# Optimization experiments

Hardware: AMD Instinct MI355X
Metric: run time of the kernel (lower is better)

The kernel has to match this reference:

```python
import jax, jax.numpy as jnp
import numpy as np

DIM = 2048
DIM_HEADS = 64
NUM_HEADS = DIM // DIM_HEADS  # 32


def setup_inputs() -> dict:
    key = jax.random.key(0)
    k1, k2, k3, k4 = jax.random.split(key, 4)
    B, N = 2, 2048
    x = jax.random.normal(k1, (B, N, DIM), dtype=jnp.float32)
    freqs = jax.random.normal(k2, (N, DIM_HEADS), dtype=jnp.float32)
    W_qkv = jax.random.normal(k3, (3 * DIM, DIM), dtype=jnp.float32) * 0.02
    W_out = jax.random.normal(k4, (DIM, DIM), dtype=jnp.float32) * 0.02
    return {"x": x, "freqs": freqs, "W_qkv": W_qkv, "W_out": W_out}


def _rotate_half(x):
    # split last dim into two halves (j=2), return cat(-x2, x1)
    x1, x2 = jnp.split(x, 2, axis=-1)
    return jnp.concatenate([-x2, x1], axis=-1)


def _apply_rotary_pos_emb(t, freqs, scale=1.0):
    # t: [b, h, n, d]; freqs: [n, rot_dim]; rotary math in float32
    out_dtype = t.dtype
    rot_dim = freqs.shape[-1]
    seq_len = t.shape[-2]
    freqs = freqs.astype(jnp.float32)[-seq_len:, :]  # [n, rot_dim]
    t = t.astype(jnp.float32)
    t_rot, t_unrot = t[..., :rot_dim], t[..., rot_dim:]
    t_rot = t_rot * jnp.cos(freqs) * scale + _rotate_half(t_rot) * jnp.sin(freqs) * scale
    return jnp.concatenate([t_rot.astype(out_dtype), t_unrot.astype(out_dtype)], axis=-1)


def reference(x, freqs, W_qkv, W_out):
    B, N, _ = x.shape
    h, d = NUM_HEADS, DIM_HEADS
    # fused QKV projection (Linear, no bias): x @ W_qkv.T
    qkv = jnp.einsum('bnc,fc->bnf', x, W_qkv)  # [B, N, 3*DIM]
    q, k, v = jnp.split(qkv, 3, axis=-1)
    q = q.reshape(B, N, h, d).transpose(0, 2, 1, 3)  # [B, h, N, d]
    k = k.reshape(B, N, h, d).transpose(0, 2, 1, 3)
    v = v.reshape(B, N, h, d).transpose(0, 2, 1, 3)
    # equal q/k seq lens -> ratio = 1, same freqs for both
    q = _apply_rotary_pos_emb(q, freqs)
    k = _apply_rotary_pos_emb(k, freqs)
    # scaled dot-product attention (non-causal)
    scale = 1.0 / np.sqrt(d).astype(np.float32)
    scores = jnp.einsum('bhqd,bhkd->bhqk', q, k) * scale
    attn = jax.nn.softmax(scores, axis=-1)
    out = jnp.einsum('bhqk,bhkd->bhqd', attn, v)
    out = out.transpose(0, 2, 1, 3).reshape(B, N, h * d)  # [B, N, DIM]
    return jnp.einsum('bnc,oc->bno', out, W_out)
```

## Files before the change

### kernel.cpp

```cpp
#include <hip/hip_runtime.h>

#define DIMC 2048
#define NSEQ 2048
#define NBATCH 2
#define NH 32
#define DH 64
#define BHEADS (NBATCH*NH)
#define MROWS (NBATCH*NSEQ)
#define NQKV (3*DIMC)

typedef __attribute__((ext_vector_type(8))) short short8;
typedef __attribute__((ext_vector_type(4))) float f32x4;
typedef __attribute__((ext_vector_type(4))) unsigned int uint4v;
typedef __attribute__((ext_vector_type(2))) unsigned int u32x2;

static __device__ __forceinline__ unsigned short f2bf(float f) {
  union { float f; unsigned int u; } v; v.f = f;
  unsigned int r = (v.u + 0x7FFFu + ((v.u >> 16) & 1u)) >> 16;
  return (unsigned short)r;
}

static __device__ __forceinline__ unsigned int cvt_pk_bf16(float lo, float hi) {
  unsigned int r;
  asm("v_cvt_pk_bf16_f32 %0, %1, %2" : "=v"(r) : "v"(lo), "v"(hi));
  return r;
}

#define BAR()    __builtin_amdgcn_s_barrier()
#define FENCE()  asm volatile("" ::: "memory")
#define LGKM0()  asm volatile("s_waitcnt lgkmcnt(0)" ::: "memory")
#define VM(n)    asm volatile("s_waitcnt vmcnt(" #n ")" ::: "memory")

__global__ __launch_bounds__(256) void cvt_bf16(const float* __restrict__ in,
                                                unsigned short* __restrict__ out,
                                                int n8) {
  int i = blockIdx.x * blockDim.x + threadIdx.x;
  int stride = gridDim.x * blockDim.x;
  for (; i < n8; i += stride) {
    const float4* p = (const float4*)in + (size_t)i * 2;
    float4 a = p[0], b = p[1];
    union { unsigned short u[8]; uint4v v; } o;
    o.u[0] = f2bf(a.x); o.u[1] = f2bf(a.y); o.u[2] = f2bf(a.z); o.u[3] = f2bf(a.w);
    o.u[4] = f2bf(b.x); o.u[5] = f2bf(b.y); o.u[6] = f2bf(b.z); o.u[7] = f2bf(b.w);
    *((uint4v*)out + i) = o.v;
  }
}

__global__ __launch_bounds__(256) void build_cs(const float* __restrict__ freqs,
                                                float2* __restrict__ cs, int n) {
  int i = blockIdx.x * blockDim.x + threadIdx.x;
  if (i < n) { float f = freqs[i]; cs[i] = make_float2(cosf(f), sinf(f)); }
}

#define QSCALE 0.18033688011112042f
#define SLOT 24576

template<int EPI>
__global__ __launch_bounds__(512, 1) void gemm128(
    const unsigned short* __restrict__ A,
    const unsigned short* __restrict__ Bm,
    int Kdim, int Ncols,
    float* __restrict__ Cout,
    unsigned short* __restrict__ qo, unsigned short* __restrict__ ko,
    unsigned short* __restrict__ vo, const float2* __restrict__ cs)
{
  extern __shared__ char Lds[];
  const int t = threadIdx.x;
  const int w = t >> 6, lane = t & 63, lr = lane & 15, g = lane >> 4;
  const int wm = w >> 2, wn = w & 3;

  const int nx = gridDim.x;
  int orig = blockIdx.y * nx + blockIdx.x;
  int cpx = (nx * gridDim.y) >> 3;
  int id = (orig & 7) * cpx + (orig >> 3);
  const int m0 = (id / nx) * 128;
  const int n0 = (id % nx) * 256;

  const int rowt = t >> 2, colt = (t & 3) * 8;
  const unsigned short* Abase = A + (size_t)(m0 + rowt) * Kdim + colt;
  const unsigned short* Bbase = Bm + (size_t)(n0 + rowt) * Kdim + colt;
  char* dstw = Lds + w * 1024;

  auto STAGE = [&](int sbuf, int T) {
    const unsigned short* sa = Abase + T * 32;
    const unsigned short* sb = Bbase + T * 32;
    __builtin_amdgcn_global_load_lds(
        (const __attribute__((address_space(1))) void*)sa,
        (__attribute__((address_space(3))) void*)(dstw + sbuf), 16, 0, 0);
    __builtin_amdgcn_global_load_lds(
        (const __attribute__((address_space(1))) void*)sb,
        (__attribute__((address_space(3))) void*)(dstw + sbuf + 8192), 16, 0, 0);
    __builtin_amdgcn_global_load_lds(
        (const __attribute__((address_space(1))) void*)(sb + (size_t)128 * Kdim),
        (__attribute__((address_space(3))) void*)(dstw + sbuf + 16384), 16, 0, 0);
  };

  short8 Af[4], Bf[4];
  auto LDAB = [&](int rb) {
    const char* ap = Lds + rb + (wm * 64 + lr) * 64 + g * 16;
    const char* bp = Lds + rb + 8192 + (wn * 64 + lr) * 64 + g * 16;
    #pragma unroll
    for (int m = 0; m < 4; m++) Af[m] = *(const short8*)(ap + m * 1024);
    #pragma unroll
    for (int n = 0; n < 4; n++) Bf[n] = *(const short8*)(bp + n * 1024);
  };

  f32x4 acc[4][4];
  f32x4 zero = {0.0f, 0.0f, 0.0f, 0.0f};
  #pragma unroll
  for (int i = 0; i < 4; i++)
    #pragma unroll
    for (int j = 0; j < 4; j++) acc[i][j] = zero;

  STAGE(0, 0); STAGE(SLOT, 1);
  VM(3);
  BAR(); FENCE();

  const int NT = Kdim >> 5;
  int rb = 0, sb = 2 * SLOT;
  for (int i = 0; i < NT; i++) {
    LDAB(rb);
    if (i + 2 < NT) STAGE(sb, i + 2);
    BAR(); LGKM0();
    __builtin_amdgcn_s_setprio(1);
    #pragma unroll
    for (int m = 0; m < 4; m++)
      #pragma unroll
      for (int n = 0; n < 4; n++)
        acc[m][n] = __builtin_amdgcn_mfma_f32_16x16x32_bf16(Af[m], Bf[n], acc[m][n], 0, 0, 0);
    __builtin_amdgcn_s_setprio(0);
    if (i < NT - 2) { VM(3); } else { VM(0); }
    BAR(); FENCE();
    rb += SLOT; if (rb == 3 * SLOT) rb = 0;
    sb += SLOT; if (sb == 3 * SLOT) sb = 0;
  }

  if (EPI == 0) {
    #pragma unroll
    for (int m = 0; m < 4; m++) {
      #pragma unroll
      for (int r = 0; r < 4; r++) {
        int row = m0 + wm * 64 + m * 16 + g * 4 + r;
        #pragma unroll
        for (int n = 0; n < 4; n++)
          Cout[(size_t)row * Ncols + (n0 + wn * 64 + n * 16 + lr)] = acc[m][n][r];
      }
    }
  } else {
    const int which = n0 >> 11;
    const int head = ((n0 & 2047) + wn * 64) >> 6;
    #pragma unroll
    for (int m = 0; m < 4; m++) {
      #pragma unroll
      for (int r = 0; r < 4; r++) {
        int row = m0 + wm * 64 + m * 16 + g * 4 + r;
        int b = row >> 11, ntok = row & 2047;
        size_t obase = ((size_t)(b * NH + head) * NSEQ + ntok) * DH;
        #pragma unroll
        for (int n = 0; n < 4; n++) {
          int d = n * 16 + lr;
          float val = acc[m][n][r];
          if (which == 2) {
            vo[obase + d] = f2bf(val);
          } else {
            float other = acc[m][n ^ 2][r];
            float2 c2 = cs[ntok * DH + d];
            float rot = (d < 32) ? (val * c2.x - other * c2.y)
                                 : (val * c2.x + other * c2.y);
            if (which == 0) qo[obase + d] = f2bf(rot * QSCALE);
            else            ko[obase + d] = f2bf(rot);
          }
        }
      }
    }
  }
}

__global__ __launch_bounds__(256, 4) void attn_fa(
    const unsigned short* __restrict__ qb,
    const unsigned short* __restrict__ kb,
    const unsigned short* __restrict__ vb,
    unsigned short* __restrict__ aob)
{
  __shared__ __align__(16) unsigned short Kl[64 * 64];
  __shared__ __align__(16) unsigned short Vt[64 * 72];
  __shared__ __align__(16) unsigned short Pl[4][32 * 72];

  const int t = threadIdx.x;
  const int w = t >> 6, lane = t & 63, lr = lane & 15, g = lane >> 4;
  const int bh = blockIdx.y;
  const int q0 = blockIdx.x * 128 + w * 32;
  const size_t hbase = (size_t)bh * NSEQ * DH;

  short8 qf[2][2];
  #pragma unroll
  for (int qt = 0; qt < 2; qt++)
    #pragma unroll
    for (int hf = 0; hf < 2; hf++)
      qf[qt][hf] = *(const short8*)(qb + hbase + (size_t)(q0 + qt * 16 + lr) * DH + hf * 32 + g * 8);

  f32x4 zero = {0.0f, 0.0f, 0.0f, 0.0f};
  f32x4 oacc[2][4];
  #pragma unroll
  for (int qt = 0; qt < 2; qt++)
    #pragma unroll
    for (int dv = 0; dv < 4; dv++) oacc[qt][dv] = zero;
  float mrun[2] = {-1e30f, -1e30f};
  float lrun[2] = {0.0f, 0.0f};

  int kro[2], kdo_[2];
  #pragma unroll
  for (int c = 0; c < 2; c++) {
    int b = w * 2048 + c * 1024 + lane * 16;
    int row = b >> 7;
    int off = b ^ ((row & 7) << 4);
    kro[c] = row;
    kdo_[c] = (off >> 1) & 63;
  }
  const int vr0 = (t & 31) * 2;
  const int vhv = (t >> 5) * 8;

  unsigned short* prow0 = &Pl[w][lr * 72];
  unsigned short* prow1 = &Pl[w][(16 + lr) * 72];

  for (int kv0 = 0; kv0 < NSEQ; kv0 += 64) {
    __syncthreads();
    #pragma unroll
    for (int c = 0; c < 2; c++) {
      const unsigned short* src = kb + hbase + (size_t)(kv0 + kro[c]) * DH + kdo_[c];
      __builtin_amdgcn_global_load_lds(
          (const __attribute__((address_space(1))) void*)src,
          (__attribute__((address_space(3))) void*)(Kl + w * 1024 + c * 512), 16, 0, 0);
    }
    {
      const unsigned short* s0 = vb + hbase + (size_t)(kv0 + vr0) * DH + vhv;
      short8 v0 = *(const short8*)(s0);
      short8 v1 = *(const short8*)(s0 + DH);
      #pragma unroll
      for (int j = 0; j < 8; j++) {
        unsigned int p = ((unsigned short)v0[j]) | (((unsigned int)(unsigned short)v1[j]) << 16);
        *(unsigned int*)&Vt[(vhv + j) * 72 + vr0] = p;
      }
    }
    __syncthreads();

    f32x4 s[2][4];
    #pragma unroll
    for (int kt = 0; kt < 4; kt++) {
      int row = kt * 16 + lr;
      int sw = (row & 7) << 4;
      int byteA = (row * 128 + g * 16) ^ sw;
      int byteB = (row * 128 + 64 + g * 16) ^ sw;
      short8 kA = *(const short8*)((const char*)Kl + byteA);
      short8 kB = *(const short8*)((const char*)Kl + byteB);
      #pragma unroll
      for (int qt = 0; qt < 2; qt++) {
        f32x4 a0 = __builtin_amdgcn_mfma_f32_16x16x32_bf16(kA, qf[qt][0], zero, 0, 0, 0);
        s[qt][kt] = __builtin_amdgcn_mfma_f32_16x16x32_bf16(kB, qf[qt][1], a0, 0, 0, 0);
      }
    }

    float nm[2];
    #pragma unroll
    for (int qt = 0; qt < 2; qt++) {
      f32x4 m01 = s[qt][0];
      #pragma unroll
      for (int kt = 1; kt < 4; kt++) {
        f32x4 sv = s[qt][kt];
        m01[0] = fmaxf(m01[0], sv[0]); m01[1] = fmaxf(m01[1], sv[1]);
        m01[2] = fmaxf(m01[2], sv[2]); m01[3] = fmaxf(m01[3], sv[3]);
      }
      float v = fmaxf(fmaxf(m01[0], m01[1]), fmaxf(m01[2], m01[3]));
      v = fmaxf(v, __shfl_xor(v, 16));
      v = fmaxf(v, __shfl_xor(v, 32));
      nm[qt] = v;
    }

    if (!__all(fmaxf(nm[0] - mrun[0], nm[1] - mrun[1]) <= 8.0f)) {
      const int sb = (lane & 48) + ((lane & 48) >> 2);
      #pragma unroll
      for (int qt = 0; qt < 2; qt++) {
        float m2 = fmaxf(mrun[qt], nm[qt]);
        float cc = exp2f(mrun[qt] - m2);
        mrun[qt] = m2;
        lrun[qt] *= cc;
        float c0r = __shfl(cc, sb + 0);
        float c1r = __shfl(cc, sb + 1);
        float c2r = __shfl(cc, sb + 2);
        float c3r = __shfl(cc, sb + 3);
        #pragma unroll
        for (int dv = 0; dv < 4; dv++) {
          f32x4 a = oacc[qt][dv];
          a[0] *= c0r; a[1] *= c1r; a[2] *= c2r; a[3] *= c3r;
          oacc[qt][dv] = a;
        }
      }
    }

    #pragma unroll
    for (int qt = 0; qt < 2; qt++) {
      float mq = mrun[qt];
      float ls = 0.0f;
      unsigned short* prow = qt ? prow1 : prow0;
      #pragma unroll
      for (int kt = 0; kt < 4; kt++) {
        f32x4 sv = s[qt][kt];
        float p0 = exp2f(sv[0] - mq), p1 = exp2f(sv[1] - mq);
        float p2 = exp2f(sv[2] - mq), p3 = exp2f(sv[3] - mq);
        ls += (p0 + p1) + (p2 + p3);
        u32x2 uu;
        uu.x = cvt_pk_bf16(p0, p1);
        uu.y = cvt_pk_bf16(p2, p3);
        *(u32x2*)(prow + kt * 16 + g * 4) = uu;
      }
      ls += __shfl_xor(ls, 16);
      ls += __shfl_xor(ls, 32);
      lrun[qt] += ls;
    }

    #pragma unroll
    for (int c0 = 0; c0 < 2; c0++) {
      short8 pa0 = *(const short8*)(prow0 + c0 * 32 + g * 8);
      short8 pa1 = *(const short8*)(prow1 + c0 * 32 + g * 8);
      #pragma unroll
      for (int dv = 0; dv < 4; dv++) {
        short8 vf = *(const short8*)&Vt[(dv * 16 + lr) * 72 + c0 * 32 + g * 8];
        oacc[0][dv] = __builtin_amdgcn_mfma_f32_16x16x32_bf16(pa0, vf, oacc[0][dv], 0, 0, 0);
        oacc[1][dv] = __builtin_amdgcn_mfma_f32_16x16x32_bf16(pa1, vf, oacc[1][dv], 0, 0, 0);
      }
    }
  }

  const int b = bh >> 5, h = bh & 31;
  const int sb = (lane & 48) + ((lane & 48) >> 2);
  #pragma unroll
  for (int qt = 0; qt < 2; qt++) {
    float inv = 1.0f / lrun[qt];
    float ir[4];
    ir[0] = __shfl(inv, sb + 0);
    ir[1] = __shfl(inv, sb + 1);
    ir[2] = __shfl(inv, sb + 2);
    ir[3] = __shfl(inv, sb + 3);
    #pragma unroll
    for (int r = 0; r < 4; r++) {
      int ntok = q0 + qt * 16 + g * 4 + r;
      size_t ob = ((size_t)(b * NSEQ + ntok)) * DIMC + h * DH;
      #pragma unroll
      for (int dv = 0; dv < 4; dv++)
        aob[ob + dv * 16 + lr] = f2bf(oacc[qt][dv][r] * ir[r]);
    }
  }
}

extern "C" void kernel_launch(void* const* d_in, const int* in_sizes, int n_in,
                              void* d_out, int out_size, void* d_ws, size_t ws_size,
                              hipStream_t stream) {
  const float* x     = (const float*)d_in[0];
  const float* freqs = (const float*)d_in[1];
  const float* Wqkv  = (const float*)d_in[2];
  const float* Wout  = (const float*)d_in[3];
  float* out = (float*)d_out;

  char* ws = (char*)d_ws;
  size_t off = 0;
  auto alloc = [&](size_t bytes) {
    void* p = ws + off;
    off += (bytes + 255) & ~(size_t)255;
    return p;
  };
  unsigned short* xb    = (unsigned short*)alloc((size_t)MROWS * DIMC * 2);
  unsigned short* wqkvb = (unsigned short*)alloc((size_t)NQKV * DIMC * 2);
  unsigned short* woutb = (unsigned short*)alloc((size_t)DIMC * DIMC * 2);
  unsigned short* qbuf  = (unsigned short*)alloc((size_t)BHEADS * NSEQ * DH * 2);
  unsigned short* kbuf  = (unsigned short*)alloc((size_t)BHEADS * NSEQ * DH * 2);
  unsigned short* vbuf  = (unsigned short*)alloc((size_t)BHEADS * NSEQ * DH * 2);
  float2* cst           = (float2*)alloc((size_t)NSEQ * DH * sizeof(float2));
  unsigned short* aob   = xb;

  (void)hipFuncSetAttribute((const void*)gemm128<1>,
      hipFuncAttributeMaxDynamicSharedMemorySize, 3 * SLOT);
  (void)hipFuncSetAttribute((const void*)gemm128<0>,
      hipFuncAttributeMaxDynamicSharedMemorySize, 3 * SLOT);

  cvt_bf16<<<2048, 256, 0, stream>>>(x, xb, MROWS * DIMC / 8);
  cvt_bf16<<<2048, 256, 0, stream>>>(Wqkv, wqkvb, NQKV * DIMC / 8);
  cvt_bf16<<<1024, 256, 0, stream>>>(Wout, woutb, DIMC * DIMC / 8);
  build_cs<<<(NSEQ * DH + 255) / 256, 256, 0, stream>>>(freqs, cst, NSEQ * DH);

  gemm128<1><<<dim3(NQKV / 256, MROWS / 128), 512, 3 * SLOT, stream>>>(
      xb, wqkvb, DIMC, NQKV, nullptr, qbuf, kbuf, vbuf, cst);

  attn_fa<<<dim3(NSEQ / 128, BHEADS), 256, 0, stream>>>(qbuf, kbuf, vbuf, aob);

  gemm128<0><<<dim3(DIMC / 256, MROWS / 128), 512, 3 * SLOT, stream>>>(
      aob, woutb, DIMC, DIMC, out, nullptr, nullptr, nullptr, nullptr);
}
```

Measured before the change: 339.1 us.

## Double-buffer GEMM register fragments, add fourth LDS stage, swizzle LDS and pad P

The GEMM main loop moves from a 3-slot to a 4-slot LDS ring. It is unrolled by two with ping-pong register fragments, so the LDS reads for the next K-step are issued before the current MFMAs, with a partial lgkmcnt wait. The global-to-LDS column placement is XOR-swizzled and matched on the read side to cut LDS bank conflicts. The attention kernel's P scratch row stride is padded from 72 to 76 elements. The cost is more LDS per block and more fragment registers.

```diff
diff --git a/kernel.cpp b/kernel.cpp
--- a/kernel.cpp
+++ b/kernel.cpp
@@ -29,6 +29,7 @@
 #define BAR()    __builtin_amdgcn_s_barrier()
 #define FENCE()  asm volatile("" ::: "memory")
 #define LGKM0()  asm volatile("s_waitcnt lgkmcnt(0)" ::: "memory")
+#define LGKM8()  asm volatile("s_waitcnt lgkmcnt(8)" ::: "memory")
 #define VM(n)    asm volatile("s_waitcnt vmcnt(" #n ")" ::: "memory")
 
 __global__ __launch_bounds__(256) void cvt_bf16(const float* __restrict__ in,
@@ -68,6 +69,7 @@
   const int t = threadIdx.x;
   const int w = t >> 6, lane = t & 63, lr = lane & 15, g = lane >> 4;
   const int wm = w >> 2, wn = w & 3;
+  const int gxs = (g * 16) ^ (((lr >> 1) & 3) << 4);
 
   const int nx = gridDim.x;
   int orig = blockIdx.y * nx + blockIdx.x;
@@ -76,7 +78,8 @@
   const int m0 = (id / nx) * 128;
   const int n0 = (id % nx) * 256;
 
-  const int rowt = t >> 2, colt = (t & 3) * 8;
+  const int rowt = t >> 2;
+  const int colt = (((t & 3) ^ ((t >> 3) & 3))) * 8;
   const unsigned short* Abase = A + (size_t)(m0 + rowt) * Kdim + colt;
   const unsigned short* Bbase = Bm + (size_t)(n0 + rowt) * Kdim + colt;
   char* dstw = Lds + w * 1024;
@@ -95,10 +98,10 @@
         (__attribute__((address_space(3))) void*)(dstw + sbuf + 16384), 16, 0, 0);
   };
 
-  short8 Af[4], Bf[4];
-  auto LDAB = [&](int rb) {
-    const char* ap = Lds + rb + (wm * 64 + lr) * 64 + g * 16;
-    const char* bp = Lds + rb + 8192 + (wn * 64 + lr) * 64 + g * 16;
+  short8 AfE[4], BfE[4], AfO[4], BfO[4];
+  auto LDAB = [&](short8 (&Af)[4], short8 (&Bf)[4], int rb) {
+    const char* ap = Lds + rb + (wm * 64 + lr) * 64 + gxs;
+    const char* bp = Lds + rb + 8192 + (wn * 64 + lr) * 64 + gxs;
     #pragma unroll
     for (int m = 0; m < 4; m++) Af[m] = *(const short8*)(ap + m * 1024);
     #pragma unroll
@@ -112,27 +115,45 @@
     #pragma unroll
     for (int j = 0; j < 4; j++) acc[i][j] = zero;
 
+  auto MM = [&](short8 (&Af)[4], short8 (&Bf)[4]) {
+    __builtin_amdgcn_s_setprio(1);
+    #pragma unroll
+    for (int m = 0; m < 4; m++)
+      #pragma unroll
+      for (int n = 0; n < 4; n++)
+        acc[m][n] = __builtin_amdgcn_mfma_f32_16x16x32_bf16(Af[m], Bf[n], acc[m][n], 0, 0, 0);
+    __builtin_amdgcn_s_setprio(0);
+  };
+
+  const int NT = Kdim >> 5;
+
   STAGE(0, 0); STAGE(SLOT, 1);
   VM(3);
   BAR(); FENCE();
-
-  const int NT = Kdim >> 5;
-  int rb = 0, sb = 2 * SLOT;
-  for (int i = 0; i < NT; i++) {
-    LDAB(rb);
-    if (i + 2 < NT) STAGE(sb, i + 2);
-    BAR(); LGKM0();
-    __builtin_amdgcn_s_setprio(1);
-    #pragma unroll
-    for (int m = 0; m < 4; m++)
-      #pragma unroll
-      for (int n = 0; n < 4; n++)
-        acc[m][n] = __builtin_amdgcn_mfma_f32_16x16x32_bf16(Af[m], Bf[n], acc[m][n], 0, 0, 0);
-    __builtin_amdgcn_s_setprio(0);
-    if (i < NT - 2) { VM(3); } else { VM(0); }
+  LDAB(AfE, BfE, 0);
+  STAGE(2 * SLOT, 2);
+  VM(3);
+  BAR(); FENCE();
+
+  int rs = SLOT;
+  int ss = 3 * SLOT;
+  for (int i = 0; i < NT; i += 2) {
+    if (i + 1 < NT) LDAB(AfO, BfO, rs);
+    if (i + 3 < NT) STAGE(ss, i + 3);
+    if (i + 1 < NT) { LGKM8(); } else { LGKM0(); }
+    MM(AfE, BfE);
+    if (i + 3 < NT) { VM(3); } else if (i + 2 < NT) { VM(0); }
     BAR(); FENCE();
-    rb += SLOT; if (rb == 3 * SLOT) rb = 0;
-    sb += SLOT; if (sb == 3 * SLOT) sb = 0;
+    rs += SLOT; if (rs == 4 * SLOT) rs = 0;
+    ss += SLOT; if (ss == 4 * SLOT) ss = 0;
+    if (i + 2 < NT) LDAB(AfE, BfE, rs);
+    if (i + 4 < NT) STAGE(ss, i + 4);
+    if (i + 2 < NT) { LGKM8(); } else { LGKM0(); }
+    MM(AfO, BfO);
+    if (i + 4 < NT) { VM(3); } else if (i + 3 < NT) { VM(0); }
+    BAR(); FENCE();
+    rs += SLOT; if (rs == 4 * SLOT) rs = 0;
+    ss += SLOT; if (ss == 4 * SLOT) ss = 0;
   }
 
   if (EPI == 0) {
@@ -184,7 +205,7 @@
 {
   __shared__ __align__(16) unsigned short Kl[64 * 64];
   __shared__ __align__(16) unsigned short Vt[64 * 72];
-  __shared__ __align__(16) unsigned short Pl[4][32 * 72];
+  __shared__ __align__(16) unsigned short Pl[4][32 * 76];
 
   const int t = threadIdx.x;
   const int w = t >> 6, lane = t & 63, lr = lane & 15, g = lane >> 4;
@@ -220,8 +241,8 @@
   const int vr0 = (t & 31) * 2;
   const int vhv = (t >> 5) * 8;
 
-  unsigned short* prow0 = &Pl[w][lr * 72];
-  unsigned short* prow1 = &Pl[w][(16 + lr) * 72];
+  unsigned short* prow0 = &Pl[w][lr * 76];
+  unsigned short* prow1 = &Pl[w][(16 + lr) * 76];
 
   for (int kv0 = 0; kv0 < NSEQ; kv0 += 64) {
     __syncthreads();
@@ -378,20 +399,20 @@
   unsigned short* aob   = xb;
 
   (void)hipFuncSetAttribute((const void*)gemm128<1>,
-      hipFuncAttributeMaxDynamicSharedMemorySize, 3 * SLOT);
+      hipFuncAttributeMaxDynamicSharedMemorySize, 4 * SLOT);
   (void)hipFuncSetAttribute((const void*)gemm128<0>,
-      hipFuncAttributeMaxDynamicSharedMemorySize, 3 * SLOT);
+      hipFuncAttributeMaxDynamicSharedMemorySize, 4 * SLOT);
 
   cvt_bf16<<<2048, 256, 0, stream>>>(x, xb, MROWS * DIMC / 8);
   cvt_bf16<<<2048, 256, 0, stream>>>(Wqkv, wqkvb, NQKV * DIMC / 8);
   cvt_bf16<<<1024, 256, 0, stream>>>(Wout, woutb, DIMC * DIMC / 8);
   build_cs<<<(NSEQ * DH + 255) / 256, 256, 0, stream>>>(freqs, cst, NSEQ * DH);
 
-  gemm128<1><<<dim3(NQKV / 256, MROWS / 128), 512, 3 * SLOT, stream>>>(
+  gemm128<1><<<dim3(NQKV / 256, MROWS / 128), 512, 4 * SLOT, stream>>>(
       xb, wqkvb, DIMC, NQKV, nullptr, qbuf, kbuf, vbuf, cst);
 
   attn_fa<<<dim3(NSEQ / 128, BHEADS), 256, 0, stream>>>(qbuf, kbuf, vbuf, aob);
 
-  gemm128<0><<<dim3(DIMC / 256, MROWS / 128), 512, 3 * SLOT, stream>>>(
+  gemm128<0><<<dim3(DIMC / 256, MROWS / 128), 512, 4 * SLOT, stream>>>(
       aob, woutb, DIMC, DIMC, out, nullptr, nullptr, nullptr, nullptr);
 }
```

New measurement: 374.8 us. +10.5%, slower.
